# Kernel optimization log

Measured on AMD Instinct MI355X. Metric: run time of the kernel, lower is better.

Reference implementation:

```python
import jax, jax.numpy as jnp
import numpy as np

B, IN_C, H, W = 32, 256, 32, 32
C_OUT, NUM_MODES, NEG_MODES, EMB = 256, 1, 3, 512
SIGMA, BETA, NEG_SCOPE, EPS = 0.5, 0.3, 2.0, 1e-12


def _l2norm(v, axis):
    return v / jnp.maximum(jnp.linalg.norm(v, axis=axis, keepdims=True), EPS)


def setup_inputs() -> dict:
    key = jax.random.key(0)
    ks = jax.random.split(key, 6)
    x = jax.random.normal(ks[0], (B, IN_C, H, W), jnp.float32)
    W_emb = jax.random.normal(ks[1], (EMB, IN_C), jnp.float32) * 0.02  # 1x1 conv kernel
    # rep_fc / neg_rep_fc: nn.Linear(1, C*modes*E), normal_init std=0.01
    rep_w = jax.random.normal(ks[2], (C_OUT * NUM_MODES * EMB, 1), jnp.float32) * 0.01
    rep_b = jax.random.normal(ks[3], (C_OUT * NUM_MODES * EMB,), jnp.float32) * 0.01
    neg_rep_w = jax.random.normal(ks[4], (C_OUT * NEG_MODES * EMB, 1), jnp.float32) * 0.01
    neg_rep_b = jax.random.normal(ks[5], (C_OUT * NEG_MODES * EMB,), jnp.float32) * 0.01
    return {"x": x, "W_emb": W_emb, "rep_w": rep_w, "rep_b": rep_b,
            "neg_rep_w": neg_rep_w, "neg_rep_b": neg_rep_b}


def reference(x, W_emb, rep_w, rep_b, neg_rep_w, neg_rep_b):
    # emb_module: 1x1 conv, then L2-normalize over channel dim (dim=1)
    emb = jnp.einsum('bchw,ec->behw', x, W_emb)
    emb = _l2norm(emb, axis=1)                                    # [B,E,H,W], unit-norm over E
    # training branch: reps = normalize(rep_fc(1.0)) = normalize(w*1 + b)
    reps = _l2norm((rep_w[:, 0] + rep_b).reshape(C_OUT, NUM_MODES, EMB), axis=2)
    reps_neg = _l2norm((neg_rep_w[:, 0] + neg_rep_b).reshape(C_OUT, NEG_MODES, EMB), axis=2)

    def dist(r):
        # ||e - r||^2 = ||e||^2 + ||r||^2 - 2 e.r = 2 - 2 e.r (both unit-norm)
        dot = jnp.einsum('behw,cme->bcmhw', emb, r)               # [B,C,M,H,W]
        return jnp.sqrt(jnp.maximum(2.0 - 2.0 * dot, 0.0))

    distances = dist(reps)                                        # [B,C,1,H,W]
    distances_neg = dist(reps_neg)                                # [B,C,3,H,W]
    inv2s2 = 1.0 / (2.0 * SIGMA ** 2)

    probs_neg = jnp.exp(-distances_neg ** 2 * inv2s2)
    cls_score_neg = probs_neg.max(axis=2)                         # [B,C,H,W]
    probs_ori = jnp.exp(-distances ** 2 * inv2s2).max(axis=2)     # [B,C,H,W]

    neg_min = distances_neg.min(axis=2, keepdims=True)            # [B,C,1,H,W]
    probs = jnp.exp(-(distances + BETA * jax.nn.relu(NEG_SCOPE - neg_min)) ** 2 * inv2s2)
    # cls_norm=True branch
    probs_sumj = probs.sum(axis=2)                                # [B,C,H,W]
    cls_score = probs_sumj / probs_sumj.sum(axis=1, keepdims=True)
    return (cls_score, cls_score_neg, distances, distances_neg, probs_ori)
```

## Files before the change

kernel.cpp:

```cpp
#include <hip/hip_runtime.h>
#include <stdint.h>

using s16x8 = __attribute__((ext_vector_type(8))) short;
using f32x4 = __attribute__((ext_vector_type(4))) float;

#define HW 1024
#define INC 256
#define EMB 512
#define NPX 32768

#define OFF_CS 0
#define OFF_CN 8388608
#define OFF_D  16777216
#define OFF_DN 25165824
#define OFF_PO 50331648

__device__ __forceinline__ uint32_t f2bf(float f) {
  uint32_t u = __float_as_uint(f);
  return (u + 0x7FFFu + ((u >> 16) & 1u)) >> 16;
}
__device__ __forceinline__ int lswz(int row, int byte) {
  return byte ^ (((row >> 2) & 7) << 4);
}
__device__ __forceinline__ void gload16(const void* g, void* l) {
  __builtin_amdgcn_global_load_lds((const __attribute__((address_space(1))) uint32_t*)g,
                                   (__attribute__((address_space(3))) uint32_t*)l, 16, 0, 0);
}

__global__ __launch_bounds__(64) void k_prep(
    const float* __restrict__ rep_w, const float* __restrict__ rep_b,
    const float* __restrict__ neg_w, const float* __restrict__ neg_b,
    uint16_t* __restrict__ R) {
  int rb = blockIdx.x, lane = threadIdx.x;
  int c = rb >> 2, md = rb & 3;
  const float* w  = (md == 0) ? rep_w : neg_w;
  const float* bb = (md == 0) ? rep_b : neg_b;
  int base = (md == 0) ? c * EMB : (c * 3 + md - 1) * EMB;
  float v[8]; float ss = 0.f;
#pragma unroll
  for (int j = 0; j < 8; ++j) {
    float t = w[base + lane * 8 + j] + bb[base + lane * 8 + j];
    v[j] = t; ss += t * t;
  }
#pragma unroll
  for (int o = 1; o < 64; o <<= 1) ss += __shfl_xor(ss, o, 64);
  float inv = 1.f / fmaxf(sqrtf(ss), 1e-12f);
  uint16_t* dst = R + rb * EMB + lane * 8;
#pragma unroll
  for (int j = 0; j < 8; ++j) dst[j] = (uint16_t)f2bf(v[j] * inv);
}

__global__ __launch_bounds__(256) void k_gemm1(
    const float* __restrict__ x, const float* __restrict__ wemb,
    uint16_t* __restrict__ emb, float* __restrict__ nparts) {
  int bid = blockIdx.x;
  int w = (bid & 7) * 128 + (bid >> 3);
  int e_tile = w & 3, px_tile = w >> 2;
  int e0 = e_tile * 128, px0 = px_tile * 128;
  int bimg = px0 >> 10, hw0 = px0 & 1023;
  int tid = threadIdx.x, lane = tid & 63, wid = tid >> 6;
  int wm = wid >> 1, wn = wid & 1, lr = lane & 15, lk = lane >> 4;
  __shared__ __align__(16) char smA[16384];
  __shared__ __align__(16) char smB[16384];
  f32x4 acc[4][4] = {};
  const float4* x4 = (const float4*)x;
  const float4* w4 = (const float4*)wemb;
  for (int kt = 0; kt < INC; kt += 64) {
    if (kt) __syncthreads();
#pragma unroll
    for (int i = 0; i < 4; ++i) {
      int p = tid + i * 256;
      int c2 = p >> 5, px4 = p & 31;
      int gi = ((bimg * INC + kt + c2 * 2) * HW + hw0) >> 2;
      float4 fa = x4[gi + px4];
      float4 fb = x4[gi + 256 + px4];
      float fa_[4] = {fa.x, fa.y, fa.z, fa.w};
      float fb_[4] = {fb.x, fb.y, fb.z, fb.w};
#pragma unroll
      for (int j = 0; j < 4; ++j) {
        int px = px4 * 4 + j;
        uint32_t val = f2bf(fa_[j]) | (f2bf(fb_[j]) << 16);
        *(uint32_t*)(smA + px * 128 + lswz(px, c2 * 4)) = val;
      }
    }
#pragma unroll
    for (int i = 0; i < 8; ++i) {
      int q = tid + i * 256;
      int er = q >> 4, c4 = q & 15;
      float4 f = w4[(((e0 + er) * INC + kt) >> 2) + c4];
      uint2 val;
      val.x = f2bf(f.x) | (f2bf(f.y) << 16);
      val.y = f2bf(f.z) | (f2bf(f.w) << 16);
      *(uint2*)(smB + er * 128 + lswz(er, c4 * 8)) = val;
    }
    __syncthreads();
#pragma unroll
    for (int kk = 0; kk < 64; kk += 32) {
      s16x8 a[4], b[4];
#pragma unroll
      for (int mi = 0; mi < 4; ++mi) {
        int row = wm * 64 + mi * 16 + lr;
        a[mi] = *(const s16x8*)(smA + row * 128 + lswz(row, (kk + lk * 8) * 2));
      }
#pragma unroll
      for (int ni = 0; ni < 4; ++ni) {
        int row = wn * 64 + ni * 16 + lr;
        b[ni] = *(const s16x8*)(smB + row * 128 + lswz(row, (kk + lk * 8) * 2));
      }
#pragma unroll
      for (int mi = 0; mi < 4; ++mi)
#pragma unroll
        for (int ni = 0; ni < 4; ++ni)
          acc[mi][ni] = __builtin_amdgcn_mfma_f32_16x16x32_bf16(a[mi], b[ni], acc[mi][ni], 0, 0, 0);
    }
  }
#pragma unroll
  for (int mi = 0; mi < 4; ++mi) {
#pragma unroll
    for (int r = 0; r < 4; ++r) {
      int pxg = px0 + wm * 64 + mi * 16 + lk * 4 + r;
      float ss = 0.f;
#pragma unroll
      for (int ni = 0; ni < 4; ++ni) {
        float v = acc[mi][ni][r];
        ss += v * v;
        uint32_t bf = f2bf(v);
        uint32_t other = (uint32_t)__shfl_xor((int)bf, 1, 64);
        if (!(lane & 1)) {
          int e = e0 + wn * 64 + ni * 16 + lr;
          *(uint32_t*)(emb + pxg * EMB + e) = bf | (other << 16);
        }
      }
      ss += __shfl_xor(ss, 1, 64);
      ss += __shfl_xor(ss, 2, 64);
      ss += __shfl_xor(ss, 4, 64);
      ss += __shfl_xor(ss, 8, 64);
      if (lr == 0) nparts[(e_tile * 2 + wn) * NPX + pxg] = ss;
    }
  }
}

__global__ __launch_bounds__(256) void k_gemm2(
    const uint16_t* __restrict__ Rm, const uint16_t* __restrict__ emb,
    const float* __restrict__ nparts, float* __restrict__ out,
    float* __restrict__ psum_part) {
  int bid = blockIdx.x;
  int w = (bid & 7) * 256 + (bid >> 3);
  int px_tile = w >> 3, rep_tile = w & 7;
  int px0 = px_tile * 128, r0 = rep_tile * 128;
  int bimg = px0 >> 10;
  int tid = threadIdx.x, lane = tid & 63, wid = tid >> 6;
  int wm = wid >> 1, wn = wid & 1, lr = lane & 15, lk = lane >> 4;
  __shared__ __align__(16) char smA[16384];
  __shared__ __align__(16) char smB[16384];
  f32x4 acc[4][4] = {};
  const char* Rb = (const char*)Rm;
  const char* Eb = (const char*)emb;
  int rowq = lane >> 3;
  int byteq = (lane & 7) * 16;
  for (int kt = 0; kt < EMB; kt += 64) {
    if (kt) __syncthreads();
#pragma unroll
    for (int i = 0; i < 4; ++i) {
      int chunk = wid + i * 4;
      int row = chunk * 8 + rowq;
      int sb = byteq ^ (((row >> 2) & 7) << 4);
      gload16(Rb + (r0 + row) * 1024 + kt * 2 + sb, smA + chunk * 1024);
      gload16(Eb + (px0 + row) * 1024 + kt * 2 + sb, smB + chunk * 1024);
    }
    __syncthreads();
#pragma unroll
    for (int kk = 0; kk < 64; kk += 32) {
      s16x8 a[4], b[4];
#pragma unroll
      for (int mi = 0; mi < 4; ++mi) {
        int row = wm * 64 + mi * 16 + lr;
        a[mi] = *(const s16x8*)(smA + row * 128 + lswz(row, (kk + lk * 8) * 2));
      }
#pragma unroll
      for (int ni = 0; ni < 4; ++ni) {
        int row = wn * 64 + ni * 16 + lr;
        b[ni] = *(const s16x8*)(smB + row * 128 + lswz(row, (kk + lk * 8) * 2));
      }
#pragma unroll
      for (int mi = 0; mi < 4; ++mi)
#pragma unroll
        for (int ni = 0; ni < 4; ++ni)
          acc[mi][ni] = __builtin_amdgcn_mfma_f32_16x16x32_bf16(a[mi], b[ni], acc[mi][ni], 0, 0, 0);
    }
  }
  __syncthreads();
  char* ep = smA + wid * 1184;
  int hwbase = (px0 & 1023) + wn * 64;
  int obase = (bimg * 256) * HW + hwbase;
  float invn[4], psacc[4];
#pragma unroll
  for (int ni = 0; ni < 4; ++ni) {
    int px = px0 + wn * 64 + ni * 16 + lr;
    float s = 0.f;
#pragma unroll
    for (int t = 0; t < 8; ++t) s += nparts[t * NPX + px];
    invn[ni] = rsqrtf(fmaxf(s, 1e-24f));
    psacc[ni] = 0.f;
  }
#pragma unroll
  for (int mi = 0; mi < 4; ++mi) {
    int clsl = wm * 16 + mi * 4 + lk;
    int cls = (r0 >> 2) + clsl;
    float pl[7][4];
#pragma unroll
    for (int ni = 0; ni < 4; ++ni) {
      float in = invn[ni];
      float d0 = acc[mi][ni][0] * in;
      float d1 = acc[mi][ni][1] * in;
      float d2 = acc[mi][ni][2] * in;
      float d3 = acc[mi][ni][3] * in;
      float q0 = fmaxf(2.f - 2.f * d0, 0.f);
      float q1 = fmaxf(2.f - 2.f * d1, 0.f);
      float q2 = fmaxf(2.f - 2.f * d2, 0.f);
      float q3 = fmaxf(2.f - 2.f * d3, 0.f);
      float dist0 = sqrtf(q0);
      float qmin = fminf(q1, fminf(q2, q3));
      float negmin = sqrtf(qmin);
      float pen = 0.3f * fmaxf(2.f - negmin, 0.f);
      float tt = dist0 + pen;
      float probs = __expf(-2.f * tt * tt);
      pl[0][ni] = probs;
      pl[1][ni] = __expf(-2.f * qmin);
      pl[2][ni] = dist0;
      pl[3][ni] = sqrtf(q1);
      pl[4][ni] = sqrtf(q2);
      pl[5][ni] = sqrtf(q3);
      pl[6][ni] = __expf(-2.f * q0);
      psacc[ni] += probs;
    }
    int bc = obase + cls * HW;
    int bn = OFF_DN + (bimg * 768 + cls * 3) * HW + hwbase;
    int pbase[7] = { OFF_CS + bc, OFF_CN + bc, OFF_D + bc,
                     bn, bn + HW, bn + 2 * HW, OFF_PO + bc };
#pragma unroll
    for (int p = 0; p < 7; ++p) {
#pragma unroll
      for (int ni = 0; ni < 4; ++ni)
        *(float*)(ep + lk * 288 + (ni * 16 + lr) * 4) = pl[p][ni];
      float4 v = *(const float4*)(ep + lk * 288 + lr * 16);
      *(float4*)(&out[pbase[p] + 4 * lr]) = v;
    }
  }
#pragma unroll
  for (int ni = 0; ni < 4; ++ni) {
    float s = psacc[ni];
    s += __shfl_xor(s, 16, 64);
    s += __shfl_xor(s, 32, 64);
    if (lk == 0)
      psum_part[(rep_tile * 2 + wm) * NPX + px0 + wn * 64 + ni * 16 + lr] = s;
  }
}

__global__ __launch_bounds__(256) void k_norm(float* __restrict__ out,
                                              const float* __restrict__ psum_part) {
  int idx4 = blockIdx.x * 256 + threadIdx.x;
  int base = idx4 << 2;
  int b = base >> 18, hw = base & 1023;
  int pxb = (b << 10) | hw;
  float sx = 0.f, sy = 0.f, sz = 0.f, sw = 0.f;
#pragma unroll
  for (int t = 0; t < 16; ++t) {
    float4 p = *(const float4*)&psum_part[t * NPX + pxb];
    sx += p.x; sy += p.y; sz += p.z; sw += p.w;
  }
  float4* o4 = (float4*)out;
  float4 v = o4[idx4];
  v.x /= sx; v.y /= sy; v.z /= sz; v.w /= sw;
  o4[idx4] = v;
}

extern "C" void kernel_launch(void* const* d_in, const int* in_sizes, int n_in,
                              void* d_out, int out_size, void* d_ws, size_t ws_size,
                              hipStream_t stream) {
  (void)in_sizes; (void)n_in; (void)out_size; (void)ws_size;
  const float* x     = (const float*)d_in[0];
  const float* wemb  = (const float*)d_in[1];
  const float* rep_w = (const float*)d_in[2];
  const float* rep_b = (const float*)d_in[3];
  const float* neg_w = (const float*)d_in[4];
  const float* neg_b = (const float*)d_in[5];
  float* out = (float*)d_out;
  char* ws = (char*)d_ws;
  uint16_t* R         = (uint16_t*)ws;
  float*    nparts    = (float*)(ws + (1 << 20));
  float*    psum_part = (float*)(ws + (2 << 20));
  uint16_t* emb       = (uint16_t*)(ws + (4 << 20));
  hipLaunchKernelGGL(k_prep,  dim3(1024), dim3(64),  0, stream,
                     rep_w, rep_b, neg_w, neg_b, R);
  hipLaunchKernelGGL(k_gemm1, dim3(1024), dim3(256), 0, stream, x, wemb, emb, nparts);
  hipLaunchKernelGGL(k_gemm2, dim3(2048), dim3(256), 0, stream, R, emb, nparts, out, psum_part);
  hipLaunchKernelGGL(k_norm,  dim3(8192), dim3(256), 0, stream, out, psum_part);
}
```

Before: 376.4 us.

## Load GEMM2 operands directly from global memory and precompute inverse class sums

The second GEMM no longer stages the rep and embedding tiles through LDS with global_load_lds and barriers. Each wave now reads its MFMA fragments straight from global memory, so the work leans on L1/L2 cache hits and frees most of the shared memory, which may raise occupancy. A new small kernel reduces the 16 partial class sums once per pixel into reciprocals. The normalization pass then does a single multiply instead of re-reading 16 partials for each output element. Risks are uncoalesced 16-byte global reads, redundant operand traffic across waves, and one extra launch.

```diff
diff --git a/kernel.cpp b/kernel.cpp
--- a/kernel.cpp
+++ b/kernel.cpp
@@ -21,10 +21,6 @@
 }
 __device__ __forceinline__ int lswz(int row, int byte) {
   return byte ^ (((row >> 2) & 7) << 4);
-}
-__device__ __forceinline__ void gload16(const void* g, void* l) {
-  __builtin_amdgcn_global_load_lds((const __attribute__((address_space(1))) uint32_t*)g,
-                                   (__attribute__((address_space(3))) uint32_t*)l, 16, 0, 0);
 }
 
 __global__ __launch_bounds__(64) void k_prep(
@@ -151,46 +147,26 @@
   int bimg = px0 >> 10;
   int tid = threadIdx.x, lane = tid & 63, wid = tid >> 6;
   int wm = wid >> 1, wn = wid & 1, lr = lane & 15, lk = lane >> 4;
-  __shared__ __align__(16) char smA[16384];
-  __shared__ __align__(16) char smB[16384];
+  __shared__ __align__(16) char ep_s[4 * 1184];
   f32x4 acc[4][4] = {};
-  const char* Rb = (const char*)Rm;
-  const char* Eb = (const char*)emb;
-  int rowq = lane >> 3;
-  int byteq = (lane & 7) * 16;
-  for (int kt = 0; kt < EMB; kt += 64) {
-    if (kt) __syncthreads();
-#pragma unroll
-    for (int i = 0; i < 4; ++i) {
-      int chunk = wid + i * 4;
-      int row = chunk * 8 + rowq;
-      int sb = byteq ^ (((row >> 2) & 7) << 4);
-      gload16(Rb + (r0 + row) * 1024 + kt * 2 + sb, smA + chunk * 1024);
-      gload16(Eb + (px0 + row) * 1024 + kt * 2 + sb, smB + chunk * 1024);
-    }
-    __syncthreads();
-#pragma unroll
-    for (int kk = 0; kk < 64; kk += 32) {
-      s16x8 a[4], b[4];
-#pragma unroll
-      for (int mi = 0; mi < 4; ++mi) {
-        int row = wm * 64 + mi * 16 + lr;
-        a[mi] = *(const s16x8*)(smA + row * 128 + lswz(row, (kk + lk * 8) * 2));
-      }
-#pragma unroll
-      for (int ni = 0; ni < 4; ++ni) {
-        int row = wn * 64 + ni * 16 + lr;
-        b[ni] = *(const s16x8*)(smB + row * 128 + lswz(row, (kk + lk * 8) * 2));
-      }
-#pragma unroll
-      for (int mi = 0; mi < 4; ++mi)
-#pragma unroll
-        for (int ni = 0; ni < 4; ++ni)
-          acc[mi][ni] = __builtin_amdgcn_mfma_f32_16x16x32_bf16(a[mi], b[ni], acc[mi][ni], 0, 0, 0);
-    }
-  }
-  __syncthreads();
-  char* ep = smA + wid * 1184;
+  const char* Ab = (const char*)Rm  + (r0  + wm * 64 + lr) * 1024 + lk * 16;
+  const char* Bb = (const char*)emb + (px0 + wn * 64 + lr) * 1024 + lk * 16;
+#pragma unroll
+  for (int ks = 0; ks < 16; ++ks) {
+    s16x8 a[4], b[4];
+#pragma unroll
+    for (int mi = 0; mi < 4; ++mi)
+      a[mi] = *(const s16x8*)(Ab + mi * 16384 + ks * 64);
+#pragma unroll
+    for (int ni = 0; ni < 4; ++ni)
+      b[ni] = *(const s16x8*)(Bb + ni * 16384 + ks * 64);
+#pragma unroll
+    for (int mi = 0; mi < 4; ++mi)
+#pragma unroll
+      for (int ni = 0; ni < 4; ++ni)
+        acc[mi][ni] = __builtin_amdgcn_mfma_f32_16x16x32_bf16(a[mi], b[ni], acc[mi][ni], 0, 0, 0);
+  }
+  char* ep = ep_s + wid * 1184;
   int hwbase = (px0 & 1023) + wn * 64;
   int obase = (bimg * 256) * HW + hwbase;
   float invn[4], psacc[4];
@@ -257,21 +233,24 @@
   }
 }
 
+__global__ __launch_bounds__(256) void k_psum(const float* __restrict__ psum_part,
+                                              float* __restrict__ inv_ps) {
+  int px = blockIdx.x * 256 + threadIdx.x;
+  float s = 0.f;
+#pragma unroll
+  for (int t = 0; t < 16; ++t) s += psum_part[t * NPX + px];
+  inv_ps[px] = 1.f / s;
+}
+
 __global__ __launch_bounds__(256) void k_norm(float* __restrict__ out,
-                                              const float* __restrict__ psum_part) {
+                                              const float* __restrict__ inv_ps) {
   int idx4 = blockIdx.x * 256 + threadIdx.x;
   int base = idx4 << 2;
   int b = base >> 18, hw = base & 1023;
-  int pxb = (b << 10) | hw;
-  float sx = 0.f, sy = 0.f, sz = 0.f, sw = 0.f;
-#pragma unroll
-  for (int t = 0; t < 16; ++t) {
-    float4 p = *(const float4*)&psum_part[t * NPX + pxb];
-    sx += p.x; sy += p.y; sz += p.z; sw += p.w;
-  }
+  float4 p = *(const float4*)&inv_ps[(b << 10) | hw];
   float4* o4 = (float4*)out;
   float4 v = o4[idx4];
-  v.x /= sx; v.y /= sy; v.z /= sz; v.w /= sw;
+  v.x *= p.x; v.y *= p.y; v.z *= p.z; v.w *= p.w;
   o4[idx4] = v;
 }
 
@@ -290,10 +269,12 @@
   uint16_t* R         = (uint16_t*)ws;
   float*    nparts    = (float*)(ws + (1 << 20));
   float*    psum_part = (float*)(ws + (2 << 20));
-  uint16_t* emb       = (uint16_t*)(ws + (4 << 20));
+  float*    inv_ps    = (float*)(ws + (4 << 20));
+  uint16_t* emb       = (uint16_t*)(ws + (5 << 20));
   hipLaunchKernelGGL(k_prep,  dim3(1024), dim3(64),  0, stream,
                      rep_w, rep_b, neg_w, neg_b, R);
   hipLaunchKernelGGL(k_gemm1, dim3(1024), dim3(256), 0, stream, x, wemb, emb, nparts);
   hipLaunchKernelGGL(k_gemm2, dim3(2048), dim3(256), 0, stream, R, emb, nparts, out, psum_part);
-  hipLaunchKernelGGL(k_norm,  dim3(8192), dim3(256), 0, stream, out, psum_part);
-}
+  hipLaunchKernelGGL(k_psum,  dim3(128),  dim3(256), 0, stream, psum_part, inv_ps);
+  hipLaunchKernelGGL(k_norm,  dim3(8192), dim3(256), 0, stream, out, inv_ps);
+}
```

After: 446.6 us. 18.6% more time.
